# Kernel optimization log

Measured on AMD Instinct MI355X. Metric: run time of the kernel, lower is better.

Reference implementation:

```python
import jax, jax.numpy as jnp
import numpy as np

N_NODES = 10000
N_EDGES = 640000
IN_DIM = 128
HID = 128
N_GRAPHS = 64


def setup_inputs() -> dict:
    key = jax.random.key(0)
    ks = jax.random.split(key, 9)
    x = jax.random.normal(ks[0], (N_NODES, IN_DIM), dtype=jnp.float32)
    edge_index = jax.random.randint(ks[1], (2, N_EDGES), 0, N_NODES, dtype=jnp.int32)
    batch = jnp.sort(jax.random.randint(ks[2], (N_NODES,), 0, N_GRAPHS, dtype=jnp.int32))
    # GCNConv weights (glorot-ish init) and zero biases
    W0 = jax.random.normal(ks[3], (IN_DIM, HID), dtype=jnp.float32) / np.float32(np.sqrt(IN_DIM))
    b0 = jnp.zeros((HID,), dtype=jnp.float32)
    W1 = jax.random.normal(ks[4], (HID, HID), dtype=jnp.float32) / np.float32(np.sqrt(HID))
    b1 = jnp.zeros((HID,), dtype=jnp.float32)
    W2 = jax.random.normal(ks[5], (HID, HID), dtype=jnp.float32) / np.float32(np.sqrt(HID))
    b2 = jnp.zeros((HID,), dtype=jnp.float32)
    return {"x": x, "edge_index": edge_index, "batch": batch,
            "W0": W0, "b0": b0, "W1": W1, "b1": b1, "W2": W2, "b2": b2}


def _gcn_conv(x, src, dst, W, b, n_nodes):
    """PyG GCNConv: self-loops + symmetric normalization, then linear+bias."""
    h = x @ W  # [N, H]
    # degree of destination nodes, +1 for the added self-loop
    deg = jax.ops.segment_sum(jnp.ones((src.shape[0],), h.dtype), dst,
                              num_segments=n_nodes) + 1.0
    dis = jax.lax.rsqrt(deg)  # deg >= 1 so no inf guard needed
    # messages along real edges, normalized by dis[src]*dis[dst]
    msg = h[src] * (dis[src] * dis[dst])[:, None]  # [E, H]
    out = jax.ops.segment_sum(msg, dst, num_segments=n_nodes)
    # self-loop contribution: dis[i]^2 * h[i]
    out = out + h * (dis * dis)[:, None]
    return out + b


def reference(x, edge_index, batch, W0, b0, W1, b1, W2, b2):
    src, dst = edge_index[0], edge_index[1]
    n_nodes = x.shape[0]
    # layer 0 and 1 followed by ReLU (dropout: eval mode -> identity)
    h = _gcn_conv(x, src, dst, W0, b0, n_nodes)
    h = jax.nn.relu(h)
    h = _gcn_conv(h, src, dst, W1, b1, n_nodes)
    h = jax.nn.relu(h)
    h = _gcn_conv(h, src, dst, W2, b2, n_nodes)
    # global mean pool over batch indices
    sums = jax.ops.segment_sum(h, batch, num_segments=N_GRAPHS)  # [B, H]
    counts = jax.ops.segment_sum(jnp.ones((n_nodes,), h.dtype), batch,
                                 num_segments=N_GRAPHS)
    return sums / jnp.maximum(counts, 1.0)[:, None]
```

## Files before the change

kernel.cpp:

```cpp
#include <hip/hip_runtime.h>
#include <hip/hip_fp16.h>

#define NN 10000
#define NE 640000
#define DIM 128
#define NG 64
#define CAP 128
#define NB 625
#define BCAP 1280

typedef _Float16 f16x8 __attribute__((ext_vector_type(8)));
typedef float f32x4 __attribute__((ext_vector_type(4)));

__global__ __launch_bounds__(256) void k_init(const int* __restrict__ batch,
                                              int* __restrict__ gstart,
                                              int* __restrict__ bcur,
                                              const float* __restrict__ W0,
                                              const float* __restrict__ W1,
                                              const float* __restrict__ W2,
                                              __half* __restrict__ wh,
                                              __half* __restrict__ wl) {
    int bid = blockIdx.x, t = threadIdx.x;
    if (bid < 40) {
        int i = bid * 256 + t;
        if (i < NB) bcur[i] = 0;
        if (i >= NN) return;
        int b = batch[i];
        int prev = (i == 0) ? -1 : batch[i - 1];
        for (int g = prev + 1; g <= b; g++) gstart[g] = i;
        if (i == NN - 1)
            for (int g = b + 1; g <= NG; g++) gstart[g] = NN;
        return;
    }
    int wid = bid - 40;
    int z = wid >> 6;
    int q = (wid & 63) * 256 + t;
    int c = q >> 7, k = q & 127;
    const float* W = (z == 0) ? W0 : (z == 1) ? W1 : W2;
    float v = W[k * 128 + c];
    __half h = __float2half(v);
    __half lo = __float2half(v - __half2float(h));
    wh[z * 16384 + c * 128 + k] = h;
    wl[z * 16384 + c * 128 + k] = lo;
}

__global__ __launch_bounds__(256) void k_p1(const int* __restrict__ ei,
                                            int* __restrict__ bcur,
                                            int* __restrict__ pk) {
    __shared__ int hist[NB];
    int t = threadIdx.x;
    for (int q = t; q < NB; q += 256) hist[q] = 0;
    __syncthreads();

    int4 s4[4], d4[4];
    int ebase = blockIdx.x * 4096;
#pragma unroll
    for (int q = 0; q < 4; q++) {
        int e = ebase + q * 1024 + t * 4;
        if (e < NE) {
            s4[q] = *(const int4*)&ei[e];
            d4[q] = *(const int4*)&ei[NE + e];
            atomicAdd(&hist[d4[q].x >> 4], 1);
            atomicAdd(&hist[d4[q].y >> 4], 1);
            atomicAdd(&hist[d4[q].z >> 4], 1);
            atomicAdd(&hist[d4[q].w >> 4], 1);
        }
    }
    __syncthreads();

    for (int q = t; q < NB; q += 256) {
        int h = hist[q];
        hist[q] = (h > 0) ? atomicAdd(&bcur[q], h) : 0;
    }
    __syncthreads();

#pragma unroll
    for (int q = 0; q < 4; q++) {
        int e = ebase + q * 1024 + t * 4;
        if (e < NE) {
            int b0 = d4[q].x >> 4, b1 = d4[q].y >> 4, b2 = d4[q].z >> 4, b3 = d4[q].w >> 4;
            int r0 = atomicAdd(&hist[b0], 1);
            int r1 = atomicAdd(&hist[b1], 1);
            int r2 = atomicAdd(&hist[b2], 1);
            int r3 = atomicAdd(&hist[b3], 1);
            if (r0 < BCAP) pk[b0 * BCAP + r0] = s4[q].x | ((d4[q].x & 15) << 14);
            if (r1 < BCAP) pk[b1 * BCAP + r1] = s4[q].y | ((d4[q].y & 15) << 14);
            if (r2 < BCAP) pk[b2 * BCAP + r2] = s4[q].z | ((d4[q].z & 15) << 14);
            if (r3 < BCAP) pk[b3 * BCAP + r3] = s4[q].w | ((d4[q].w & 15) << 14);
        }
    }
}

__global__ __launch_bounds__(256) void k_p2(const int* __restrict__ bcur,
                                            const int* __restrict__ pk,
                                            int* __restrict__ deg,
                                            int* __restrict__ csrc) {
    __shared__ int buf[16 * CAP];
    __shared__ int cnt[16];
    int b = blockIdx.x, t = threadIdx.x;
    if (t < 16) cnt[t] = 0;
    __syncthreads();

    int n = bcur[b];
    if (n > BCAP) n = BCAP;
    const int* pb = &pk[b * BCAP];
    for (int i = t; i < n; i += 256) {
        int v = pb[i];
        int nd = v >> 14;
        int slot = atomicAdd(&cnt[nd], 1);
        if (slot < CAP) buf[(nd << 7) + slot] = v & 0x3FFF;
    }
    __syncthreads();

    int node0 = b << 4;
    if (t < 16) deg[node0 + t] = cnt[t];
    int4* d4 = (int4*)&csrc[node0 << 7];
    const int4* s4 = (const int4*)buf;
#pragma unroll
    for (int i = 0; i < 2; i++) d4[t + i * 256] = s4[t + i * 256];
}

__global__ __launch_bounds__(256) void k_gemm(const float* __restrict__ in,
                                              const __half* __restrict__ whT,
                                              const __half* __restrict__ wlT,
                                              const int* __restrict__ deg,
                                              __half* __restrict__ g16, int relu) {
    int t = threadIdx.x;
    int w = t >> 6, l = t & 63;
    int rw = blockIdx.x * 32 + (w & 1) * 16;
    int cw = blockIdx.y * 64 + (w >> 1) * 32;
    int lr = l & 15, lg = l >> 4;
    int row = rw + lr;
    int rclamp = min(row, NN - 1);
    const _Float16* wh = (const _Float16*)whT;
    const _Float16* wl = (const _Float16*)wlT;
    f32x4 acc0 = {0.f, 0.f, 0.f, 0.f}, acc1 = {0.f, 0.f, 0.f, 0.f};
#pragma unroll
    for (int ks = 0; ks < 4; ks++) {
        int kb = ks * 32 + lg * 8;
        float4 xa = *(const float4*)&in[rclamp * 128 + kb];
        float4 xb = *(const float4*)&in[rclamp * 128 + kb + 4];
        float x0 = xa.x, x1 = xa.y, x2 = xa.z, x3 = xa.w;
        float x4 = xb.x, x5 = xb.y, x6 = xb.z, x7 = xb.w;
        if (relu) {
            x0 = fmaxf(x0, 0.f); x1 = fmaxf(x1, 0.f); x2 = fmaxf(x2, 0.f); x3 = fmaxf(x3, 0.f);
            x4 = fmaxf(x4, 0.f); x5 = fmaxf(x5, 0.f); x6 = fmaxf(x6, 0.f); x7 = fmaxf(x7, 0.f);
        }
        f16x8 ah, al;
        ah[0] = (_Float16)x0; al[0] = (_Float16)(x0 - (float)ah[0]);
        ah[1] = (_Float16)x1; al[1] = (_Float16)(x1 - (float)ah[1]);
        ah[2] = (_Float16)x2; al[2] = (_Float16)(x2 - (float)ah[2]);
        ah[3] = (_Float16)x3; al[3] = (_Float16)(x3 - (float)ah[3]);
        ah[4] = (_Float16)x4; al[4] = (_Float16)(x4 - (float)ah[4]);
        ah[5] = (_Float16)x5; al[5] = (_Float16)(x5 - (float)ah[5]);
        ah[6] = (_Float16)x6; al[6] = (_Float16)(x6 - (float)ah[6]);
        ah[7] = (_Float16)x7; al[7] = (_Float16)(x7 - (float)ah[7]);
        int c0 = cw + lr;
        f16x8 bh0 = *(const f16x8*)&wh[c0 * 128 + kb];
        f16x8 bl0 = *(const f16x8*)&wl[c0 * 128 + kb];
        f16x8 bh1 = *(const f16x8*)&wh[(c0 + 16) * 128 + kb];
        f16x8 bl1 = *(const f16x8*)&wl[(c0 + 16) * 128 + kb];
        acc0 = __builtin_amdgcn_mfma_f32_16x16x32_f16(ah, bh0, acc0, 0, 0, 0);
        acc1 = __builtin_amdgcn_mfma_f32_16x16x32_f16(ah, bh1, acc1, 0, 0, 0);
        acc0 = __builtin_amdgcn_mfma_f32_16x16x32_f16(al, bh0, acc0, 0, 0, 0);
        acc1 = __builtin_amdgcn_mfma_f32_16x16x32_f16(al, bh1, acc1, 0, 0, 0);
        acc0 = __builtin_amdgcn_mfma_f32_16x16x32_f16(ah, bl0, acc0, 0, 0, 0);
        acc1 = __builtin_amdgcn_mfma_f32_16x16x32_f16(ah, bl1, acc1, 0, 0, 0);
    }
#pragma unroll
    for (int reg = 0; reg < 4; reg++) {
        int r = rw + lg * 4 + reg;
        if (r < NN) {
            float d = rsqrtf((float)deg[r] + 1.0f);
            int c = cw + lr;
            g16[r * 128 + c] = __float2half(acc0[reg] * d);
            g16[r * 128 + c + 16] = __float2half(acc1[reg] * d);
        }
    }
}

__global__ __launch_bounds__(256) void k_agg(const __half2* __restrict__ gp,
                                             const float* __restrict__ bias,
                                             const int* __restrict__ deg,
                                             const int* __restrict__ csrc,
                                             float* __restrict__ out) {
    int wid = blockIdx.x * 4 + (threadIdx.x >> 6);
    int lane = threadIdx.x & 63;
    if (wid >= NN) return;
    int i = wid;
    int dgi = __builtin_amdgcn_readfirstlane(deg[i]);
    int n = min(dgi, CAP);
    int e0 = i << 7;
    float2 f0 = __half22float2(gp[i * 64 + lane]);
    float ax = f0.x, ay = f0.y;
    float bx = 0.f, by = 0.f;
    float cx = 0.f, cy = 0.f;
    float dx = 0.f, dy = 0.f;
    for (int base = 0; base < n; base += 64) {
        int m = n - base;
        if (m > 64) m = 64;
        int myedge = (lane < m) ? csrc[e0 + base + lane] : 0;
        int j = 0;
        for (; j + 15 < m; j += 16) {
            int s0 = __builtin_amdgcn_readlane(myedge, j);
            int s1 = __builtin_amdgcn_readlane(myedge, j + 1);
            int s2 = __builtin_amdgcn_readlane(myedge, j + 2);
            int s3 = __builtin_amdgcn_readlane(myedge, j + 3);
            int s4 = __builtin_amdgcn_readlane(myedge, j + 4);
            int s5 = __builtin_amdgcn_readlane(myedge, j + 5);
            int s6 = __builtin_amdgcn_readlane(myedge, j + 6);
            int s7 = __builtin_amdgcn_readlane(myedge, j + 7);
            int s8 = __builtin_amdgcn_readlane(myedge, j + 8);
            int s9 = __builtin_amdgcn_readlane(myedge, j + 9);
            int s10 = __builtin_amdgcn_readlane(myedge, j + 10);
            int s11 = __builtin_amdgcn_readlane(myedge, j + 11);
            int s12 = __builtin_amdgcn_readlane(myedge, j + 12);
            int s13 = __builtin_amdgcn_readlane(myedge, j + 13);
            int s14 = __builtin_amdgcn_readlane(myedge, j + 14);
            int s15 = __builtin_amdgcn_readlane(myedge, j + 15);
            float2 v0 = __half22float2(gp[s0 * 64 + lane]);
            float2 v1 = __half22float2(gp[s1 * 64 + lane]);
            float2 v2 = __half22float2(gp[s2 * 64 + lane]);
            float2 v3 = __half22float2(gp[s3 * 64 + lane]);
            float2 v4 = __half22float2(gp[s4 * 64 + lane]);
            float2 v5 = __half22float2(gp[s5 * 64 + lane]);
            float2 v6 = __half22float2(gp[s6 * 64 + lane]);
            float2 v7 = __half22float2(gp[s7 * 64 + lane]);
            float2 v8 = __half22float2(gp[s8 * 64 + lane]);
            float2 v9 = __half22float2(gp[s9 * 64 + lane]);
            float2 v10 = __half22float2(gp[s10 * 64 + lane]);
            float2 v11 = __half22float2(gp[s11 * 64 + lane]);
            float2 v12 = __half22float2(gp[s12 * 64 + lane]);
            float2 v13 = __half22float2(gp[s13 * 64 + lane]);
            float2 v14 = __half22float2(gp[s14 * 64 + lane]);
            float2 v15 = __half22float2(gp[s15 * 64 + lane]);
            ax += v0.x; ay += v0.y;  bx += v1.x; by += v1.y;
            cx += v2.x; cy += v2.y;  dx += v3.x; dy += v3.y;
            ax += v4.x; ay += v4.y;  bx += v5.x; by += v5.y;
            cx += v6.x; cy += v6.y;  dx += v7.x; dy += v7.y;
            ax += v8.x; ay += v8.y;  bx += v9.x; by += v9.y;
            cx += v10.x; cy += v10.y; dx += v11.x; dy += v11.y;
            ax += v12.x; ay += v12.y; bx += v13.x; by += v13.y;
            cx += v14.x; cy += v14.y; dx += v15.x; dy += v15.y;
        }
        for (; j < m; j++) {
            int s0 = __builtin_amdgcn_readlane(myedge, j);
            float2 v0 = __half22float2(gp[s0 * 64 + lane]);
            ax += v0.x; ay += v0.y;
        }
    }
    float di = rsqrtf((float)dgi + 1.0f);
    float2 bb = ((const float2*)bias)[lane];
    float2 o;
    o.x = di * ((ax + bx) + (cx + dx)) + bb.x;
    o.y = di * ((ay + by) + (cy + dy)) + bb.y;
    ((float2*)out)[i * 64 + lane] = o;
}

__global__ __launch_bounds__(256) void k_pool(const float* __restrict__ h,
                                              const int* __restrict__ gstart,
                                              float* __restrict__ out) {
    int g = blockIdx.x;
    int s = gstart[g], e = gstart[g + 1];
    int t = threadIdx.x;
    int c = t & 127, half = t >> 7;
    float acc = 0.f;
    for (int n = s + half; n < e; n += 2) acc += h[n * 128 + c];
    __shared__ float sm[256];
    sm[t] = acc;
    __syncthreads();
    if (half == 0) {
        float cnt = (float)max(e - s, 1);
        out[g * 128 + c] = (sm[c] + sm[128 + c]) / cnt;
    }
}

extern "C" void kernel_launch(void* const* d_in, const int* in_sizes, int n_in,
                              void* d_out, int out_size, void* d_ws, size_t ws_size,
                              hipStream_t stream) {
    const float* x     = (const float*)d_in[0];
    const int*   ei    = (const int*)d_in[1];
    const int*   batch = (const int*)d_in[2];
    const float* W0 = (const float*)d_in[3];
    const float* b0 = (const float*)d_in[4];
    const float* W1 = (const float*)d_in[5];
    const float* b1 = (const float*)d_in[6];
    const float* W2 = (const float*)d_in[7];
    const float* b2 = (const float*)d_in[8];
    float* out = (float*)d_out;

    float* ws    = (float*)d_ws;
    int*   deg   = (int*)ws;
    int*   gstart= (int*)(ws + 10240);
    int*   bcur  = (int*)(ws + 10320);
    int*   csrc  = (int*)(ws + 10960);
    __half* g16  = (__half*)(ws + 1290960);
    float* abuf  = ws + 1930960;
    int*   pk    = (int*)(ws + 1930960);
    __half* wh   = (__half*)(ws + 3210960);
    __half* wlo  = (__half*)(ws + 3235536);

    k_init<<<232, 256, 0, stream>>>(batch, gstart, bcur, W0, W1, W2, wh, wlo);
    k_p1<<<157, 256, 0, stream>>>(ei, bcur, pk);
    k_p2<<<NB, 256, 0, stream>>>(bcur, pk, deg, csrc);

    dim3 ggrid(313, 2);
    k_gemm<<<ggrid, 256, 0, stream>>>(x, wh, wlo, deg, g16, 0);
    k_agg<<<2500, 256, 0, stream>>>((const __half2*)g16, b0, deg, csrc, abuf);
    k_gemm<<<ggrid, 256, 0, stream>>>(abuf, wh + 16384, wlo + 16384, deg, g16, 1);
    k_agg<<<2500, 256, 0, stream>>>((const __half2*)g16, b1, deg, csrc, abuf);
    k_gemm<<<ggrid, 256, 0, stream>>>(abuf, wh + 32768, wlo + 32768, deg, g16, 1);
    k_agg<<<2500, 256, 0, stream>>>((const __half2*)g16, b2, deg, csrc, abuf);

    k_pool<<<NG, 256, 0, stream>>>(abuf, gstart, out);
}
```

Measured before the change: 198.4 us.

## Aggregate via LDS-resident column slices with transposed uint16 edge lists

Rewrites the aggregation so each block loads a 4-column slice of the fp16 projected features for all nodes into LDS, then each thread gathers neighbor rows from LDS instead of global memory. The GEMM epilogue writes features column-pair-major, and the CSR build stores source indices as uint16 in a transposed layout padded with a zero dummy node, plus a per-64-node max degree so lanes loop uniformly. This trades random global gathers for LDS gathers but adds redundant per-block full-slice loads (each block loads 80KB) and padding work for low-degree nodes.

```diff
diff --git a/kernel.cpp b/kernel.cpp
--- a/kernel.cpp
+++ b/kernel.cpp
@@ -2,8 +2,8 @@
 #include <hip/hip_fp16.h>
 
 #define NN 10000
+#define NNP 10016
 #define NE 640000
-#define DIM 128
 #define NG 64
 #define CAP 128
 #define NB 625
@@ -15,6 +15,7 @@
 __global__ __launch_bounds__(256) void k_init(const int* __restrict__ batch,
                                               int* __restrict__ gstart,
                                               int* __restrict__ bcur,
+                                              int* __restrict__ gmax,
                                               const float* __restrict__ W0,
                                               const float* __restrict__ W1,
                                               const float* __restrict__ W2,
@@ -24,6 +25,7 @@
     if (bid < 40) {
         int i = bid * 256 + t;
         if (i < NB) bcur[i] = 0;
+        if (i < 160) gmax[i] = 0;
         if (i >= NN) return;
         int b = batch[i];
         int prev = (i == 0) ? -1 : batch[i - 1];
@@ -94,11 +96,13 @@
 __global__ __launch_bounds__(256) void k_p2(const int* __restrict__ bcur,
                                             const int* __restrict__ pk,
                                             int* __restrict__ deg,
-                                            int* __restrict__ csrc) {
-    __shared__ int buf[16 * CAP];
+                                            int* __restrict__ gmax,
+                                            unsigned short* __restrict__ csrcT) {
+    __shared__ unsigned short buf[16 * CAP];
     __shared__ int cnt[16];
     int b = blockIdx.x, t = threadIdx.x;
     if (t < 16) cnt[t] = 0;
+    for (int q = t; q < 1024; q += 256) ((unsigned int*)buf)[q] = 10000u | (10000u << 16);
     __syncthreads();
 
     int n = bcur[b];
@@ -108,23 +112,32 @@
         int v = pb[i];
         int nd = v >> 14;
         int slot = atomicAdd(&cnt[nd], 1);
-        if (slot < CAP) buf[(nd << 7) + slot] = v & 0x3FFF;
+        if (slot < CAP) buf[(nd << 7) + slot] = (unsigned short)(v & 0x3FFF);
     }
     __syncthreads();
 
     int node0 = b << 4;
     if (t < 16) deg[node0 + t] = cnt[t];
-    int4* d4 = (int4*)&csrc[node0 << 7];
-    const int4* s4 = (const int4*)buf;
+    if (t == 0) {
+        int m = 0;
 #pragma unroll
-    for (int i = 0; i < 2; i++) d4[t + i * 256] = s4[t + i * 256];
+        for (int i = 0; i < 16; i++) m = max(m, min(cnt[i], CAP));
+        atomicMax(&gmax[node0 >> 6], m);
+    }
+    unsigned int* cT = (unsigned int*)csrcT;
+    for (int q = t; q < 1024; q += 256) {
+        int pr = q & 7, j = q >> 3;
+        unsigned int lo = buf[(pr * 2) * 128 + j];
+        unsigned int hi = buf[(pr * 2 + 1) * 128 + j];
+        cT[j * (NN / 2) + (node0 >> 1) + pr] = lo | (hi << 16);
+    }
 }
 
 __global__ __launch_bounds__(256) void k_gemm(const float* __restrict__ in,
                                               const __half* __restrict__ whT,
                                               const __half* __restrict__ wlT,
                                               const int* __restrict__ deg,
-                                              __half* __restrict__ g16, int relu) {
+                                              unsigned int* __restrict__ g16p, int relu) {
     int t = threadIdx.x;
     int w = t >> 6, l = t & 63;
     int rw = blockIdx.x * 32 + (w & 1) * 16;
@@ -167,94 +180,118 @@
         acc0 = __builtin_amdgcn_mfma_f32_16x16x32_f16(ah, bl0, acc0, 0, 0, 0);
         acc1 = __builtin_amdgcn_mfma_f32_16x16x32_f16(ah, bl1, acc1, 0, 0, 0);
     }
-#pragma unroll
-    for (int reg = 0; reg < 4; reg++) {
-        int r = rw + lg * 4 + reg;
-        if (r < NN) {
-            float d = rsqrtf((float)deg[r] + 1.0f);
-            int c = cw + lr;
-            g16[r * 128 + c] = __float2half(acc0[reg] * d);
-            g16[r * 128 + c + 16] = __float2half(acc1[reg] * d);
-        }
-    }
-}
-
-__global__ __launch_bounds__(256) void k_agg(const __half2* __restrict__ gp,
+    if (rw < NN) {
+        int4 dg = *(const int4*)&deg[rw + lg * 4];
+        float dv0 = rsqrtf((float)dg.x + 1.0f);
+        float dv1 = rsqrtf((float)dg.y + 1.0f);
+        float dv2 = rsqrtf((float)dg.z + 1.0f);
+        float dv3 = rsqrtf((float)dg.w + 1.0f);
+        float u0 = acc0[0] * dv0, u1 = acc0[1] * dv1, u2 = acc0[2] * dv2, u3 = acc0[3] * dv3;
+        float v0 = acc1[0] * dv0, v1 = acc1[1] * dv1, v2 = acc1[2] * dv2, v3 = acc1[3] * dv3;
+        float pu0 = __shfl_xor(u0, 1), pu1 = __shfl_xor(u1, 1);
+        float pu2 = __shfl_xor(u2, 1), pu3 = __shfl_xor(u3, 1);
+        float pv0 = __shfl_xor(v0, 1), pv1 = __shfl_xor(v1, 1);
+        float pv2 = __shfl_xor(v2, 1), pv3 = __shfl_xor(v3, 1);
+        if (!(lr & 1)) {
+            int r0 = rw + lg * 4;
+            int pairA = (cw + lr) >> 1;
+            int pairB = pairA + 8;
+            __half2 h;
+            uint4 A, B;
+            h = __floats2half2_rn(u0, pu0); A.x = *(unsigned int*)&h;
+            h = __floats2half2_rn(u1, pu1); A.y = *(unsigned int*)&h;
+            h = __floats2half2_rn(u2, pu2); A.z = *(unsigned int*)&h;
+            h = __floats2half2_rn(u3, pu3); A.w = *(unsigned int*)&h;
+            h = __floats2half2_rn(v0, pv0); B.x = *(unsigned int*)&h;
+            h = __floats2half2_rn(v1, pv1); B.y = *(unsigned int*)&h;
+            h = __floats2half2_rn(v2, pv2); B.z = *(unsigned int*)&h;
+            h = __floats2half2_rn(v3, pv3); B.w = *(unsigned int*)&h;
+            *(uint4*)&g16p[pairA * NN + r0] = A;
+            *(uint4*)&g16p[pairB * NN + r0] = B;
+        }
+    }
+}
+
+__device__ __forceinline__ void acc4(uint2 v, float& a, float& b, float& c, float& d) {
+    float2 f0 = __half22float2(*(__half2*)&v.x);
+    float2 f1 = __half22float2(*(__half2*)&v.y);
+    a += f0.x; b += f0.y; c += f1.x; d += f1.y;
+}
+
+__global__ __launch_bounds__(512) void k_agg(const unsigned int* __restrict__ g16p,
                                              const float* __restrict__ bias,
                                              const int* __restrict__ deg,
-                                             const int* __restrict__ csrc,
+                                             const unsigned short* __restrict__ csrcT,
+                                             const int* __restrict__ gmax,
                                              float* __restrict__ out) {
-    int wid = blockIdx.x * 4 + (threadIdx.x >> 6);
-    int lane = threadIdx.x & 63;
-    if (wid >= NN) return;
-    int i = wid;
-    int dgi = __builtin_amdgcn_readfirstlane(deg[i]);
-    int n = min(dgi, CAP);
-    int e0 = i << 7;
-    float2 f0 = __half22float2(gp[i * 64 + lane]);
-    float ax = f0.x, ay = f0.y;
-    float bx = 0.f, by = 0.f;
-    float cx = 0.f, cy = 0.f;
-    float dx = 0.f, dy = 0.f;
-    for (int base = 0; base < n; base += 64) {
-        int m = n - base;
-        if (m > 64) m = 64;
-        int myedge = (lane < m) ? csrc[e0 + base + lane] : 0;
+    extern __shared__ unsigned int lds[];
+    int bid = blockIdx.x;
+    int cs = bid >> 4, nrb = bid & 15;
+    int t = threadIdx.x;
+    const unsigned int* p0 = g16p + (cs * 2) * NN;
+    const unsigned int* p1 = g16p + (cs * 2 + 1) * NN;
+    for (int n = t; n < NN; n += 512) {
+        uint2 v; v.x = p0[n]; v.y = p1[n];
+        *(uint2*)&lds[n * 2] = v;
+    }
+    if (t < NNP - NN) {
+        uint2 z; z.x = 0u; z.y = 0u;
+        *(uint2*)&lds[(NN + t) * 2] = z;
+    }
+    __syncthreads();
+
+    float bb0 = bias[cs * 4 + 0], bb1 = bias[cs * 4 + 1];
+    float bb2 = bias[cs * 4 + 2], bb3 = bias[cs * 4 + 3];
+    int base = nrb * 640;
+    for (int dd = t; dd < 640; dd += 512) {
+        int d = base + dd;
+        if (d >= NN) break;
+        int dg = deg[d];
+        int gm = __builtin_amdgcn_readfirstlane(gmax[d >> 6]);
+        float s0, s1, s2, s3, r0 = 0.f, r1 = 0.f, r2 = 0.f, r3 = 0.f;
+        {
+            uint2 sv = *(uint2*)&lds[d * 2];
+            float2 f0 = __half22float2(*(__half2*)&sv.x);
+            float2 f1 = __half22float2(*(__half2*)&sv.y);
+            s0 = f0.x; s1 = f0.y; s2 = f1.x; s3 = f1.y;
+        }
+        const unsigned short* cp = csrcT + d;
         int j = 0;
-        for (; j + 15 < m; j += 16) {
-            int s0 = __builtin_amdgcn_readlane(myedge, j);
-            int s1 = __builtin_amdgcn_readlane(myedge, j + 1);
-            int s2 = __builtin_amdgcn_readlane(myedge, j + 2);
-            int s3 = __builtin_amdgcn_readlane(myedge, j + 3);
-            int s4 = __builtin_amdgcn_readlane(myedge, j + 4);
-            int s5 = __builtin_amdgcn_readlane(myedge, j + 5);
-            int s6 = __builtin_amdgcn_readlane(myedge, j + 6);
-            int s7 = __builtin_amdgcn_readlane(myedge, j + 7);
-            int s8 = __builtin_amdgcn_readlane(myedge, j + 8);
-            int s9 = __builtin_amdgcn_readlane(myedge, j + 9);
-            int s10 = __builtin_amdgcn_readlane(myedge, j + 10);
-            int s11 = __builtin_amdgcn_readlane(myedge, j + 11);
-            int s12 = __builtin_amdgcn_readlane(myedge, j + 12);
-            int s13 = __builtin_amdgcn_readlane(myedge, j + 13);
-            int s14 = __builtin_amdgcn_readlane(myedge, j + 14);
-            int s15 = __builtin_amdgcn_readlane(myedge, j + 15);
-            float2 v0 = __half22float2(gp[s0 * 64 + lane]);
-            float2 v1 = __half22float2(gp[s1 * 64 + lane]);
-            float2 v2 = __half22float2(gp[s2 * 64 + lane]);
-            float2 v3 = __half22float2(gp[s3 * 64 + lane]);
-            float2 v4 = __half22float2(gp[s4 * 64 + lane]);
-            float2 v5 = __half22float2(gp[s5 * 64 + lane]);
-            float2 v6 = __half22float2(gp[s6 * 64 + lane]);
-            float2 v7 = __half22float2(gp[s7 * 64 + lane]);
-            float2 v8 = __half22float2(gp[s8 * 64 + lane]);
-            float2 v9 = __half22float2(gp[s9 * 64 + lane]);
-            float2 v10 = __half22float2(gp[s10 * 64 + lane]);
-            float2 v11 = __half22float2(gp[s11 * 64 + lane]);
-            float2 v12 = __half22float2(gp[s12 * 64 + lane]);
-            float2 v13 = __half22float2(gp[s13 * 64 + lane]);
-            float2 v14 = __half22float2(gp[s14 * 64 + lane]);
-            float2 v15 = __half22float2(gp[s15 * 64 + lane]);
-            ax += v0.x; ay += v0.y;  bx += v1.x; by += v1.y;
-            cx += v2.x; cy += v2.y;  dx += v3.x; dy += v3.y;
-            ax += v4.x; ay += v4.y;  bx += v5.x; by += v5.y;
-            cx += v6.x; cy += v6.y;  dx += v7.x; dy += v7.y;
-            ax += v8.x; ay += v8.y;  bx += v9.x; by += v9.y;
-            cx += v10.x; cy += v10.y; dx += v11.x; dy += v11.y;
-            ax += v12.x; ay += v12.y; bx += v13.x; by += v13.y;
-            cx += v14.x; cy += v14.y; dx += v15.x; dy += v15.y;
-        }
-        for (; j < m; j++) {
-            int s0 = __builtin_amdgcn_readlane(myedge, j);
-            float2 v0 = __half22float2(gp[s0 * 64 + lane]);
-            ax += v0.x; ay += v0.y;
-        }
-    }
-    float di = rsqrtf((float)dgi + 1.0f);
-    float2 bb = ((const float2*)bias)[lane];
-    float2 o;
-    o.x = di * ((ax + bx) + (cx + dx)) + bb.x;
-    o.y = di * ((ay + by) + (cy + dy)) + bb.y;
-    ((float2*)out)[i * 64 + lane] = o;
+        for (; j + 8 <= gm; j += 8) {
+            int a0 = cp[(j + 0) * NN];
+            int a1 = cp[(j + 1) * NN];
+            int a2 = cp[(j + 2) * NN];
+            int a3 = cp[(j + 3) * NN];
+            int a4 = cp[(j + 4) * NN];
+            int a5 = cp[(j + 5) * NN];
+            int a6 = cp[(j + 6) * NN];
+            int a7 = cp[(j + 7) * NN];
+            uint2 v0 = *(uint2*)&lds[a0 * 2];
+            uint2 v1 = *(uint2*)&lds[a1 * 2];
+            uint2 v2 = *(uint2*)&lds[a2 * 2];
+            uint2 v3 = *(uint2*)&lds[a3 * 2];
+            uint2 v4 = *(uint2*)&lds[a4 * 2];
+            uint2 v5 = *(uint2*)&lds[a5 * 2];
+            uint2 v6 = *(uint2*)&lds[a6 * 2];
+            uint2 v7 = *(uint2*)&lds[a7 * 2];
+            acc4(v0, s0, s1, s2, s3); acc4(v1, r0, r1, r2, r3);
+            acc4(v2, s0, s1, s2, s3); acc4(v3, r0, r1, r2, r3);
+            acc4(v4, s0, s1, s2, s3); acc4(v5, r0, r1, r2, r3);
+            acc4(v6, s0, s1, s2, s3); acc4(v7, r0, r1, r2, r3);
+        }
+        for (; j < gm; j++) {
+            int a = cp[j * NN];
+            uint2 v = *(uint2*)&lds[a * 2];
+            acc4(v, s0, s1, s2, s3);
+        }
+        float di = rsqrtf((float)dg + 1.0f);
+        float4 o;
+        o.x = di * (s0 + r0) + bb0;
+        o.y = di * (s1 + r1) + bb1;
+        o.z = di * (s2 + r2) + bb2;
+        o.w = di * (s3 + r3) + bb3;
+        *(float4*)&out[d * 128 + cs * 4] = o;
+    }
 }
 
 __global__ __launch_bounds__(256) void k_pool(const float* __restrict__ h,
@@ -293,24 +330,26 @@
     int*   deg   = (int*)ws;
     int*   gstart= (int*)(ws + 10240);
     int*   bcur  = (int*)(ws + 10320);
-    int*   csrc  = (int*)(ws + 10960);
-    __half* g16  = (__half*)(ws + 1290960);
-    float* abuf  = ws + 1930960;
-    int*   pk    = (int*)(ws + 1930960);
-    __half* wh   = (__half*)(ws + 3210960);
-    __half* wlo  = (__half*)(ws + 3235536);
-
-    k_init<<<232, 256, 0, stream>>>(batch, gstart, bcur, W0, W1, W2, wh, wlo);
+    int*   gmax  = (int*)(ws + 10960);
+    unsigned short* csrcT = (unsigned short*)(ws + 11200);
+    unsigned int*   g16p  = (unsigned int*)(ws + 651200);
+    float* abuf  = ws + 1291200;
+    int*   pk    = (int*)(ws + 1291200);
+    __half* wh   = (__half*)(ws + 2571200);
+    __half* wlo  = (__half*)(ws + 2595776);
+
+    k_init<<<232, 256, 0, stream>>>(batch, gstart, bcur, gmax, W0, W1, W2, wh, wlo);
     k_p1<<<157, 256, 0, stream>>>(ei, bcur, pk);
-    k_p2<<<NB, 256, 0, stream>>>(bcur, pk, deg, csrc);
+    k_p2<<<NB, 256, 0, stream>>>(bcur, pk, deg, gmax, csrcT);
 
     dim3 ggrid(313, 2);
-    k_gemm<<<ggrid, 256, 0, stream>>>(x, wh, wlo, deg, g16, 0);
-    k_agg<<<2500, 256, 0, stream>>>((const __half2*)g16, b0, deg, csrc, abuf);
-    k_gemm<<<ggrid, 256, 0, stream>>>(abuf, wh + 16384, wlo + 16384, deg, g16, 1);
-    k_agg<<<2500, 256, 0, stream>>>((const __half2*)g16, b1, deg, csrc, abuf);
-    k_gemm<<<ggrid, 256, 0, stream>>>(abuf, wh + 32768, wlo + 32768, deg, g16, 1);
-    k_agg<<<2500, 256, 0, stream>>>((const __half2*)g16, b2, deg, csrc, abuf);
+    const size_t aggLds = (size_t)NNP * 8;
+    k_gemm<<<ggrid, 256, 0, stream>>>(x, wh, wlo, deg, g16p, 0);
+    k_agg<<<512, 512, aggLds, stream>>>(g16p, b0, deg, csrcT, gmax, abuf);
+    k_gemm<<<ggrid, 256, 0, stream>>>(abuf, wh + 16384, wlo + 16384, deg, g16p, 1);
+    k_agg<<<512, 512, aggLds, stream>>>(g16p, b1, deg, csrcT, gmax, abuf);
+    k_gemm<<<ggrid, 256, 0, stream>>>(abuf, wh + 32768, wlo + 32768, deg, g16p, 1);
+    k_agg<<<512, 512, aggLds, stream>>>(g16p, b2, deg, csrcT, gmax, abuf);
 
     k_pool<<<NG, 256, 0, stream>>>(abuf, gstart, out);
 }
```

New measurement: 214.6 us. +8.2%, slower.

## Split each aggregation wavefront into two half-waves gathering alternate edges with 8-byte loads

Applied to the files above, without the earlier changes.

The aggregation kernel now has each half of a 64-lane wavefront process alternate neighbor edges. Each lane loads 4 halves (8 bytes) per row instead of 2, and the two halves are combined with a cross-half shuffle at the end. Odd edge counts are padded with a sentinel index NN that points to a zero row, which the GEMM now writes for the padded rows, so the pair loop needs no tail branch. The intent is to double the edges in flight per wavefront and widen each gather load. In exchange the per-node neighbor cap drops from 128 to 127, and the kernel adds shuffles and an extra barrier in CSR build.

```diff
diff --git a/kernel.cpp b/kernel.cpp
--- a/kernel.cpp
+++ b/kernel.cpp
@@ -3,7 +3,6 @@
 
 #define NN 10000
 #define NE 640000
-#define DIM 128
 #define NG 64
 #define CAP 128
 #define NB 625
@@ -113,7 +112,13 @@
     __syncthreads();
 
     int node0 = b << 4;
-    if (t < 16) deg[node0 + t] = cnt[t];
+    if (t < 16) {
+        int c = cnt[t];
+        deg[node0 + t] = c;
+        buf[(t << 7) + min(c, CAP - 1)] = NN;
+    }
+    __syncthreads();
+
     int4* d4 = (int4*)&csrc[node0 << 7];
     const int4* s4 = (const int4*)buf;
 #pragma unroll
@@ -170,91 +175,96 @@
 #pragma unroll
     for (int reg = 0; reg < 4; reg++) {
         int r = rw + lg * 4 + reg;
+        int c = cw + lr;
         if (r < NN) {
             float d = rsqrtf((float)deg[r] + 1.0f);
-            int c = cw + lr;
             g16[r * 128 + c] = __float2half(acc0[reg] * d);
             g16[r * 128 + c + 16] = __float2half(acc1[reg] * d);
-        }
-    }
-}
-
-__global__ __launch_bounds__(256) void k_agg(const __half2* __restrict__ gp,
+        } else {
+            g16[r * 128 + c] = __float2half(0.f);
+            g16[r * 128 + c + 16] = __float2half(0.f);
+        }
+    }
+}
+
+__device__ __forceinline__ void accp(uint2 v, float2& p, float2& q) {
+    float2 f0 = __half22float2(*(__half2*)&v.x);
+    float2 f1 = __half22float2(*(__half2*)&v.y);
+    p.x += f0.x; p.y += f0.y; q.x += f1.x; q.y += f1.y;
+}
+
+__global__ __launch_bounds__(256) void k_agg(const __half* __restrict__ g16,
                                              const float* __restrict__ bias,
                                              const int* __restrict__ deg,
                                              const int* __restrict__ csrc,
                                              float* __restrict__ out) {
     int wid = blockIdx.x * 4 + (threadIdx.x >> 6);
-    int lane = threadIdx.x & 63;
+    int l = threadIdx.x & 63;
     if (wid >= NN) return;
     int i = wid;
     int dgi = __builtin_amdgcn_readfirstlane(deg[i]);
-    int n = min(dgi, CAP);
-    int e0 = i << 7;
-    float2 f0 = __half22float2(gp[i * 64 + lane]);
-    float ax = f0.x, ay = f0.y;
-    float bx = 0.f, by = 0.f;
-    float cx = 0.f, cy = 0.f;
-    float dx = 0.f, dy = 0.f;
-    for (int base = 0; base < n; base += 64) {
-        int m = n - base;
+    int n = min(dgi, CAP - 1);
+    int np = (n + 1) & ~1;
+    int half = l >> 5, li = l & 31;
+    int co = li * 4;
+    float2 A0 = {0.f, 0.f}, A1 = {0.f, 0.f};
+    float2 B0 = {0.f, 0.f}, B1 = {0.f, 0.f};
+    if (half == 0) {
+        uint2 sv = *(const uint2*)&g16[i * 128 + co];
+        float2 f0 = __half22float2(*(__half2*)&sv.x);
+        float2 f1 = __half22float2(*(__half2*)&sv.y);
+        A0 = f0; A1 = f1;
+    }
+    const int* cp = &csrc[i << 7];
+    for (int base = 0; base < np; base += 64) {
+        int m = np - base;
         if (m > 64) m = 64;
-        int myedge = (lane < m) ? csrc[e0 + base + lane] : 0;
+        int myedge = (l < m) ? cp[base + l] : NN;
+        int pairs = m >> 1;
         int j = 0;
-        for (; j + 15 < m; j += 16) {
-            int s0 = __builtin_amdgcn_readlane(myedge, j);
-            int s1 = __builtin_amdgcn_readlane(myedge, j + 1);
-            int s2 = __builtin_amdgcn_readlane(myedge, j + 2);
-            int s3 = __builtin_amdgcn_readlane(myedge, j + 3);
-            int s4 = __builtin_amdgcn_readlane(myedge, j + 4);
-            int s5 = __builtin_amdgcn_readlane(myedge, j + 5);
-            int s6 = __builtin_amdgcn_readlane(myedge, j + 6);
-            int s7 = __builtin_amdgcn_readlane(myedge, j + 7);
-            int s8 = __builtin_amdgcn_readlane(myedge, j + 8);
-            int s9 = __builtin_amdgcn_readlane(myedge, j + 9);
-            int s10 = __builtin_amdgcn_readlane(myedge, j + 10);
-            int s11 = __builtin_amdgcn_readlane(myedge, j + 11);
-            int s12 = __builtin_amdgcn_readlane(myedge, j + 12);
-            int s13 = __builtin_amdgcn_readlane(myedge, j + 13);
-            int s14 = __builtin_amdgcn_readlane(myedge, j + 14);
-            int s15 = __builtin_amdgcn_readlane(myedge, j + 15);
-            float2 v0 = __half22float2(gp[s0 * 64 + lane]);
-            float2 v1 = __half22float2(gp[s1 * 64 + lane]);
-            float2 v2 = __half22float2(gp[s2 * 64 + lane]);
-            float2 v3 = __half22float2(gp[s3 * 64 + lane]);
-            float2 v4 = __half22float2(gp[s4 * 64 + lane]);
-            float2 v5 = __half22float2(gp[s5 * 64 + lane]);
-            float2 v6 = __half22float2(gp[s6 * 64 + lane]);
-            float2 v7 = __half22float2(gp[s7 * 64 + lane]);
-            float2 v8 = __half22float2(gp[s8 * 64 + lane]);
-            float2 v9 = __half22float2(gp[s9 * 64 + lane]);
-            float2 v10 = __half22float2(gp[s10 * 64 + lane]);
-            float2 v11 = __half22float2(gp[s11 * 64 + lane]);
-            float2 v12 = __half22float2(gp[s12 * 64 + lane]);
-            float2 v13 = __half22float2(gp[s13 * 64 + lane]);
-            float2 v14 = __half22float2(gp[s14 * 64 + lane]);
-            float2 v15 = __half22float2(gp[s15 * 64 + lane]);
-            ax += v0.x; ay += v0.y;  bx += v1.x; by += v1.y;
-            cx += v2.x; cy += v2.y;  dx += v3.x; dy += v3.y;
-            ax += v4.x; ay += v4.y;  bx += v5.x; by += v5.y;
-            cx += v6.x; cy += v6.y;  dx += v7.x; dy += v7.y;
-            ax += v8.x; ay += v8.y;  bx += v9.x; by += v9.y;
-            cx += v10.x; cy += v10.y; dx += v11.x; dy += v11.y;
-            ax += v12.x; ay += v12.y; bx += v13.x; by += v13.y;
-            cx += v14.x; cy += v14.y; dx += v15.x; dy += v15.y;
-        }
-        for (; j < m; j++) {
-            int s0 = __builtin_amdgcn_readlane(myedge, j);
-            float2 v0 = __half22float2(gp[s0 * 64 + lane]);
-            ax += v0.x; ay += v0.y;
-        }
-    }
-    float di = rsqrtf((float)dgi + 1.0f);
-    float2 bb = ((const float2*)bias)[lane];
-    float2 o;
-    o.x = di * ((ax + bx) + (cx + dx)) + bb.x;
-    o.y = di * ((ay + by) + (cy + dy)) + bb.y;
-    ((float2*)out)[i * 64 + lane] = o;
+        for (; j + 8 <= pairs; j += 8) {
+            int r0 = __shfl(myedge, 2 * j + half);
+            int r1 = __shfl(myedge, 2 * j + 2 + half);
+            int r2 = __shfl(myedge, 2 * j + 4 + half);
+            int r3 = __shfl(myedge, 2 * j + 6 + half);
+            int r4 = __shfl(myedge, 2 * j + 8 + half);
+            int r5 = __shfl(myedge, 2 * j + 10 + half);
+            int r6 = __shfl(myedge, 2 * j + 12 + half);
+            int r7 = __shfl(myedge, 2 * j + 14 + half);
+            uint2 v0 = *(const uint2*)&g16[r0 * 128 + co];
+            uint2 v1 = *(const uint2*)&g16[r1 * 128 + co];
+            uint2 v2 = *(const uint2*)&g16[r2 * 128 + co];
+            uint2 v3 = *(const uint2*)&g16[r3 * 128 + co];
+            uint2 v4 = *(const uint2*)&g16[r4 * 128 + co];
+            uint2 v5 = *(const uint2*)&g16[r5 * 128 + co];
+            uint2 v6 = *(const uint2*)&g16[r6 * 128 + co];
+            uint2 v7 = *(const uint2*)&g16[r7 * 128 + co];
+            accp(v0, A0, A1); accp(v1, B0, B1);
+            accp(v2, A0, A1); accp(v3, B0, B1);
+            accp(v4, A0, A1); accp(v5, B0, B1);
+            accp(v6, A0, A1); accp(v7, B0, B1);
+        }
+        for (; j < pairs; j++) {
+            int r = __shfl(myedge, 2 * j + half);
+            uint2 v = *(const uint2*)&g16[r * 128 + co];
+            accp(v, A0, A1);
+        }
+    }
+    A0.x += B0.x; A0.y += B0.y; A1.x += B1.x; A1.y += B1.y;
+    A0.x += __shfl_xor(A0.x, 32);
+    A0.y += __shfl_xor(A0.y, 32);
+    A1.x += __shfl_xor(A1.x, 32);
+    A1.y += __shfl_xor(A1.y, 32);
+    if (half == 0) {
+        float di = rsqrtf((float)dgi + 1.0f);
+        float4 bb = *(const float4*)&bias[co];
+        float4 o;
+        o.x = di * A0.x + bb.x;
+        o.y = di * A0.y + bb.y;
+        o.z = di * A1.x + bb.z;
+        o.w = di * A1.y + bb.w;
+        *(float4*)&out[i * 128 + co] = o;
+    }
 }
 
 __global__ __launch_bounds__(256) void k_pool(const float* __restrict__ h,
@@ -295,10 +305,10 @@
     int*   bcur  = (int*)(ws + 10320);
     int*   csrc  = (int*)(ws + 10960);
     __half* g16  = (__half*)(ws + 1290960);
-    float* abuf  = ws + 1930960;
-    int*   pk    = (int*)(ws + 1930960);
-    __half* wh   = (__half*)(ws + 3210960);
-    __half* wlo  = (__half*)(ws + 3235536);
+    float* abuf  = ws + 1931984;
+    int*   pk    = (int*)(ws + 1931984);
+    __half* wh   = (__half*)(ws + 3211984);
+    __half* wlo  = (__half*)(ws + 3236560);
 
     k_init<<<232, 256, 0, stream>>>(batch, gstart, bcur, W0, W1, W2, wh, wlo);
     k_p1<<<157, 256, 0, stream>>>(ei, bcur, pk);
@@ -306,11 +316,11 @@
 
     dim3 ggrid(313, 2);
     k_gemm<<<ggrid, 256, 0, stream>>>(x, wh, wlo, deg, g16, 0);
-    k_agg<<<2500, 256, 0, stream>>>((const __half2*)g16, b0, deg, csrc, abuf);
+    k_agg<<<2500, 256, 0, stream>>>(g16, b0, deg, csrc, abuf);
     k_gemm<<<ggrid, 256, 0, stream>>>(abuf, wh + 16384, wlo + 16384, deg, g16, 1);
-    k_agg<<<2500, 256, 0, stream>>>((const __half2*)g16, b1, deg, csrc, abuf);
+    k_agg<<<2500, 256, 0, stream>>>(g16, b1, deg, csrc, abuf);
     k_gemm<<<ggrid, 256, 0, stream>>>(abuf, wh + 32768, wlo + 32768, deg, g16, 1);
-    k_agg<<<2500, 256, 0, stream>>>((const __half2*)g16, b2, deg, csrc, abuf);
+    k_agg<<<2500, 256, 0, stream>>>(g16, b2, deg, csrc, abuf);
 
     k_pool<<<NG, 256, 0, stream>>>(abuf, gstart, out);
 }
```

Result: no change. 197.4 us (-0.5%).
